# Kernel tuning notes

Measured on AMD Instinct MI355X. Metric: run time of the kernel, lower is better.

## Reference

```python
import jax, jax.numpy as jnp
import numpy as np

G, NPG, HID, NLAYERS, MAXZ, K = 256, 128, 256, 3, 1000, 30
N = G * NPG          # 32768 nodes
E = N * 16           # 524288 edges
TOTAL_DIM = HID * NLAYERS + 1  # 769


def setup_inputs():
    key = jax.random.key(0)
    ks = jax.random.split(key, 12)
    z = jax.random.randint(ks[0], (N,), 0, MAXZ)
    edge_index = jax.random.randint(ks[1], (2, E), 0, N)
    batch = jnp.arange(N) // NPG  # contiguous equal-size graphs
    emb = jax.random.normal(ks[2], (MAXZ, HID), jnp.float32)
    s = 1.0 / np.sqrt(HID)
    gcn_w = jax.random.normal(ks[3], (NLAYERS, HID, HID), jnp.float32) * s
    gcn_b = jnp.zeros((NLAYERS, HID), jnp.float32)
    gcn_w_last = jax.random.normal(ks[4], (HID, 1), jnp.float32) * s
    gcn_b_last = jnp.zeros((1,), jnp.float32)
    conv1_w = jax.random.normal(ks[5], (16, 1, 5), jnp.float32) * (1.0 / np.sqrt(5))
    conv1_b = jnp.zeros((16,), jnp.float32)
    conv2_w = jax.random.normal(ks[6], (32, 16, 5), jnp.float32) * (1.0 / np.sqrt(80))
    conv2_b = jnp.zeros((32,), jnp.float32)
    kd = K * TOTAL_DIM            # 23070
    flat = 32 * ((kd - 4) // 2 - 4)  # 368928
    lin1_w = jax.random.normal(ks[7], (128, flat), jnp.float32) * (1.0 / np.sqrt(flat))
    lin1_b = jnp.zeros((128,), jnp.float32)
    lin2_w = jax.random.normal(ks[8], (1, 128), jnp.float32) * (1.0 / np.sqrt(128))
    lin2_b = jnp.zeros((1,), jnp.float32)
    return dict(z=z, edge_index=edge_index, batch=batch, emb=emb, gcn_w=gcn_w,
                gcn_b=gcn_b, gcn_w_last=gcn_w_last, gcn_b_last=gcn_b_last,
                conv1_w=conv1_w, conv1_b=conv1_b, conv2_w=conv2_w, conv2_b=conv2_b,
                lin1_w=lin1_w, lin1_b=lin1_b, lin2_w=lin2_w, lin2_b=lin2_b)


def reference(z, edge_index, batch, emb, gcn_w, gcn_b, gcn_w_last, gcn_b_last,
              conv1_w, conv1_b, conv2_w, conv2_b, lin1_w, lin1_b, lin2_w, lin2_b):
    src, dst = edge_index[0], edge_index[1]
    # GCNConv normalization with self-loops: D^{-1/2}(A+I)D^{-1/2}
    deg = 1.0 + jax.ops.segment_sum(jnp.ones((E,), jnp.float32), dst, num_segments=N)
    dinv = jax.lax.rsqrt(deg)
    enorm = dinv[src] * dinv[dst]   # per-edge norm
    snorm = 1.0 / deg               # self-loop norm

    def gcn(x, W, b):
        xw = x @ W
        agg = jax.ops.segment_sum(enorm[:, None] * xw[src], dst, num_segments=N)
        return agg + snorm[:, None] * xw + b

    x = emb[z]
    xs = []
    for i in range(NLAYERS):
        x = jnp.tanh(gcn(x, gcn_w[i], gcn_b[i]))
        xs.append(x)
    xs.append(jnp.tanh(gcn(x, gcn_w_last, gcn_b_last)))
    h = jnp.concatenate(xs, axis=-1)  # [N, TOTAL_DIM]

    # global_sort_pool: per-graph descending sort by last channel, keep top-k
    hg = h.reshape(G, NPG, TOTAL_DIM)
    order = jnp.argsort(-hg[:, :, -1], axis=1)
    hg = jnp.take_along_axis(hg, order[:, :, None], axis=1)[:, :K]
    p = hg.reshape(G, 1, K * TOTAL_DIM)

    dn = ('NCH', 'OIH', 'NCH')
    c = jax.lax.conv_general_dilated(p, conv1_w, (1,), 'VALID', dimension_numbers=dn)
    c = jax.nn.relu(c + conv1_b[None, :, None])
    c = jax.lax.reduce_window(c, -jnp.inf, jax.lax.max, (1, 1, 2), (1, 1, 2), 'VALID')
    c = jax.lax.conv_general_dilated(c, conv2_w, (1,), 'VALID', dimension_numbers=dn)
    c = jax.nn.relu(c + conv2_b[None, :, None])
    f = c.reshape(G, -1)
    f = jax.nn.relu(f @ lin1_w.T + lin1_b)
    return (f @ lin2_w.T + lin2_b).reshape(-1)
```

## Files before the change

kernel.cpp:

```cpp
#include <hip/hip_runtime.h>

#define NN      32768
#define EE      524288
#define GG      256
#define NPG     128
#define HID     256
#define KTOP    30
#define TD      769
#define HSTR    772
#define PLEN    23070
#define C1LEN   23066
#define POOLLEN 11533
#define C2LEN   11529
#define FLAT    368928
#define L1_KRANGE 512
#define L1_KS   721

#define SWZ(c) ((c) + 4 * ((c) >> 5))

__global__ __launch_bounds__(256) void k_deg(const int* __restrict__ dst, int* __restrict__ deg_cnt) {
    int e = blockIdx.x * 256 + threadIdx.x;
    atomicAdd(&deg_cnt[dst[e]], 1);
}

__global__ __launch_bounds__(256) void k_norm(const int* __restrict__ deg_cnt,
                                              float* __restrict__ dinv, float* __restrict__ snorm) {
    int n = blockIdx.x * 256 + threadIdx.x;
    float dg = 1.0f + (float)deg_cnt[n];
    dinv[n] = rsqrtf(dg);
    snorm[n] = 1.0f / dg;
}

__global__ __launch_bounds__(1024) void k_scan(const int* __restrict__ deg_cnt, int* __restrict__ row_start) {
    __shared__ int sA[1024];
    int t = threadIdx.x;
    int base = t * 32;
    int s = 0;
    for (int i = 0; i < 32; i++) s += deg_cnt[base + i];
    sA[t] = s;
    __syncthreads();
    for (int off = 1; off < 1024; off <<= 1) {
        int v = (t >= off) ? sA[t - off] : 0;
        __syncthreads();
        sA[t] += v;
        __syncthreads();
    }
    int run = sA[t] - s;
    for (int i = 0; i < 32; i++) { row_start[base + i] = run; run += deg_cnt[base + i]; }
}

__global__ __launch_bounds__(256) void k_csrfill(const int* __restrict__ src, const int* __restrict__ dst,
                                                 const int* __restrict__ row_start, int* __restrict__ fill,
                                                 const float* __restrict__ dinv,
                                                 int* __restrict__ csr_src, float* __restrict__ csr_w) {
    int e = blockIdx.x * 256 + threadIdx.x;
    int s = src[e], d = dst[e];
    int pos = row_start[d] + atomicAdd(&fill[d], 1);
    csr_src[pos] = s;
    csr_w[pos] = dinv[s] * dinv[d];
}

__global__ __launch_bounds__(256) void k_embed(const int* __restrict__ z, const float* __restrict__ emb,
                                               float* __restrict__ x) {
    int i = blockIdx.x * 256 + threadIdx.x;
    int n = i >> 6, l = i & 63;
    ((float4*)x)[(size_t)n * 64 + l] = ((const float4*)emb)[(size_t)z[n] * 64 + l];
}

__global__ __launch_bounds__(256) void k_w2t(const float* __restrict__ w2, float* __restrict__ w2t_g) {
    for (int i = threadIdx.x; i < 2560; i += 256)
        w2t_g[i] = w2[(i & 31) * 80 + (i >> 5)];
}

__global__ __launch_bounds__(256) void k_gemm_gcn(const float* __restrict__ A, const float* __restrict__ B,
                                                  float* __restrict__ C) {
    __shared__ float As[16][132];
    __shared__ float Bs[16][140];
    int m0 = blockIdx.x * 128;
    int n0 = blockIdx.y * 128;
    int tid = threadIdx.x;
    int ty = tid >> 4, tx = tid & 15;
    float acc[8][8] = {};
    for (int k0 = 0; k0 < 256; k0 += 16) {
        {
            int m = tid >> 2, kq = (tid & 3) * 4;
            #pragma unroll
            for (int r = 0; r < 2; r++) {
                float4 v = *(const float4*)&A[(size_t)(m0 + m + 64 * r) * 256 + k0 + kq];
                As[kq + 0][m + 64 * r] = v.x;
                As[kq + 1][m + 64 * r] = v.y;
                As[kq + 2][m + 64 * r] = v.z;
                As[kq + 3][m + 64 * r] = v.w;
            }
            int n = (tid & 31) * 4, kk = tid >> 5;
            #pragma unroll
            for (int r = 0; r < 2; r++) {
                float4 v = *(const float4*)&B[(size_t)(k0 + kk + 8 * r) * 256 + n0 + n];
                *(float4*)&Bs[kk + 8 * r][SWZ(n)] = v;
            }
        }
        __syncthreads();
        #pragma unroll
        for (int k = 0; k < 16; k++) {
            float a[8], b[8];
            *(float4*)&a[0] = *(float4*)&As[k][ty * 8];
            *(float4*)&a[4] = *(float4*)&As[k][ty * 8 + 4];
            *(float4*)&b[0] = *(float4*)&Bs[k][SWZ(tx * 8)];
            *(float4*)&b[4] = *(float4*)&Bs[k][SWZ(tx * 8 + 4)];
            #pragma unroll
            for (int i = 0; i < 8; i++)
                #pragma unroll
                for (int j = 0; j < 8; j++) acc[i][j] += a[i] * b[j];
        }
        __syncthreads();
    }
    #pragma unroll
    for (int i = 0; i < 8; i++) {
        int m = m0 + ty * 8 + i;
        float4 v0 = make_float4(acc[i][0], acc[i][1], acc[i][2], acc[i][3]);
        float4 v1 = make_float4(acc[i][4], acc[i][5], acc[i][6], acc[i][7]);
        *(float4*)&C[(size_t)m * 256 + n0 + tx * 8] = v0;
        *(float4*)&C[(size_t)m * 256 + n0 + tx * 8 + 4] = v1;
    }
}

__global__ __launch_bounds__(256) void k_agg(const float* __restrict__ xw, const int* __restrict__ row_start,
                                             const int* __restrict__ deg_cnt, const int* __restrict__ csr_src,
                                             const float* __restrict__ csr_w, const float* __restrict__ snorm,
                                             const float* __restrict__ bias, float* __restrict__ xn,
                                             float* __restrict__ h, int hoff,
                                             const float* __restrict__ wl, float* __restrict__ xwl) {
    int d = blockIdx.x * 4 + (threadIdx.x >> 6);
    int l = threadIdx.x & 63;
    float4 v = ((const float4*)xw)[(size_t)d * 64 + l];
    float sn = snorm[d];
    float4 acc = make_float4(sn * v.x, sn * v.y, sn * v.z, sn * v.w);
    int st = row_start[d], cnt = deg_cnt[d];
    for (int j = 0; j < cnt; j++) {
        int s = csr_src[st + j];
        float w = csr_w[st + j];
        float4 u = ((const float4*)xw)[(size_t)s * 64 + l];
        acc.x += w * u.x; acc.y += w * u.y; acc.z += w * u.z; acc.w += w * u.w;
    }
    float4 b = ((const float4*)bias)[l];
    acc.x = tanhf(acc.x + b.x);
    acc.y = tanhf(acc.y + b.y);
    acc.z = tanhf(acc.z + b.z);
    acc.w = tanhf(acc.w + b.w);
    ((float4*)xn)[(size_t)d * 64 + l] = acc;
    *(float4*)&h[(size_t)d * HSTR + hoff + l * 4] = acc;
    if (wl != nullptr) {
        float4 w4 = ((const float4*)wl)[l];
        float s = acc.x * w4.x + acc.y * w4.y + acc.z * w4.z + acc.w * w4.w;
        #pragma unroll
        for (int off = 32; off; off >>= 1) s += __shfl_down(s, off, 64);
        if (l == 0) xwl[d] = s;
    }
}

__global__ __launch_bounds__(256) void k_agg_last(const float* __restrict__ xwl, const int* __restrict__ row_start,
                                                  const int* __restrict__ deg_cnt, const int* __restrict__ csr_src,
                                                  const float* __restrict__ csr_w, const float* __restrict__ snorm,
                                                  const float* __restrict__ blast, float* __restrict__ h) {
    int d = blockIdx.x * 256 + threadIdx.x;
    float acc = snorm[d] * xwl[d];
    int st = row_start[d], cnt = deg_cnt[d];
    for (int j = 0; j < cnt; j++) acc += csr_w[st + j] * xwl[csr_src[st + j]];
    h[(size_t)d * HSTR + 768] = tanhf(acc + blast[0]);
}

__global__ __launch_bounds__(128) void k_sort_gather(const float* __restrict__ h, float* __restrict__ P) {
    __shared__ float kk[128];
    __shared__ int ii[128];
    int g = blockIdx.x, t = threadIdx.x;
    kk[t] = h[(size_t)(g * 128 + t) * HSTR + 768];
    ii[t] = t;
    __syncthreads();
    for (int size = 2; size <= 128; size <<= 1) {
        for (int stride = size >> 1; stride > 0; stride >>= 1) {
            int p = t ^ stride;
            if (p > t) {
                float ka = kk[t], kbv = kk[p];
                int ia = ii[t], ib = ii[p];
                bool aFirst = (ka > kbv) || (ka == kbv && ia < ib);
                bool asc = (t & size) == 0;
                if (asc != aFirst) { kk[t] = kbv; kk[p] = ka; ii[t] = ib; ii[p] = ia; }
            }
            __syncthreads();
        }
    }
    float* Pg = P + (size_t)g * PLEN;
    for (int r = 0; r < KTOP; r++) {
        const float* srcp = h + (size_t)(g * 128 + ii[r]) * HSTR;
        for (int c = t; c < TD; c += 128) Pg[(size_t)r * TD + c] = srcp[c];
    }
}

#define JT 128
#define CONV_T 4
__global__ __launch_bounds__(256) void k_conv(const float* __restrict__ P,
                                              const float* __restrict__ w1, const float* __restrict__ b1,
                                              const float* __restrict__ w2t_g, const float* __restrict__ b2,
                                              float* __restrict__ f) {
    __shared__ float sle[136];
    __shared__ float slo[136];
    __shared__ float pool[16][136];
    __shared__ float w2t[80][33];
    __shared__ float outs[32][133];
    __shared__ float w1s[16][5];
    __shared__ float b1s[16];
    __shared__ float b2s[32];
    int g = blockIdx.x;
    int tid = threadIdx.x;
    const float* Pg = P + (size_t)g * PLEN;
    for (int i = tid; i < 2560; i += 256) w2t[i >> 5][i & 31] = w2t_g[i];
    for (int i = tid; i < 80; i += 256) w1s[i / 5][i % 5] = w1[i];
    if (tid < 16) b1s[tid] = b1[tid];
    if (tid < 32) b2s[tid] = b2[tid];

    int c2 = tid & 31;
    int jg = tid >> 5;
    size_t fg = (size_t)g * FLAT;

    for (int tt = 0; tt < CONV_T; tt++) {
        int j0 = (blockIdx.y * CONV_T + tt) * JT;
        if (j0 >= C2LEN) break;
        __syncthreads();
        for (int i = tid; i < 268; i += 256) {
            float v = Pg[min(2 * j0 + i, PLEN - 1)];
            if (i & 1) slo[i >> 1] = v; else sle[i >> 1] = v;
        }
        __syncthreads();
        for (int i = tid; i < 16 * 132; i += 256) {
            int c1 = i / 132, t = i % 132;
            float e0 = sle[t], o0 = slo[t], e1 = sle[t + 1], o1 = slo[t + 1], e2 = sle[t + 2], o2 = slo[t + 2];
            float u0 = w1s[c1][0], u1 = w1s[c1][1], u2 = w1s[c1][2], u3 = w1s[c1][3], u4 = w1s[c1][4];
            float a = b1s[c1] + u0 * e0 + u1 * o0 + u2 * e1 + u3 * o1 + u4 * e2;
            float b = b1s[c1] + u0 * o0 + u1 * e1 + u2 * o1 + u3 * e2 + u4 * o2;
            pool[c1][t] = fmaxf(fmaxf(a, b), 0.0f);
        }
        __syncthreads();
        float acc[16];
        float bb = b2s[c2];
        #pragma unroll
        for (int jj = 0; jj < 16; jj++) acc[jj] = bb;
        int jbase = jg * 16;
        for (int c1 = 0; c1 < 16; c1++) {
            float p[20];
            #pragma unroll
            for (int q = 0; q < 5; q++) {
                float4 v = *(float4*)&pool[c1][jbase + q * 4];
                p[q * 4 + 0] = v.x; p[q * 4 + 1] = v.y; p[q * 4 + 2] = v.z; p[q * 4 + 3] = v.w;
            }
            float wk[5];
            #pragma unroll
            for (int k = 0; k < 5; k++) wk[k] = w2t[c1 * 5 + k][c2];
            #pragma unroll
            for (int k = 0; k < 5; k++)
                #pragma unroll
                for (int jj = 0; jj < 16; jj++) acc[jj] += wk[k] * p[jj + k];
        }
        #pragma unroll
        for (int jj = 0; jj < 16; jj++) outs[c2][jbase + jj] = fmaxf(acc[jj], 0.0f);
        __syncthreads();
        for (int it = 0; it < 16; it++) {
            int i = tid + it * 256;
            int cc = i >> 7, j = (i & 127) + j0;
            if (j < C2LEN) f[fg + (size_t)cc * C2LEN + j] = outs[cc][i & 127];
        }
    }
}

__global__ __launch_bounds__(256) void k_lin1(const float* __restrict__ f, const float* __restrict__ W,
                                              float* __restrict__ partial) {
    __shared__ float As[16][132];
    __shared__ float Bs[16][140];
    int m0 = blockIdx.x * 128;
    int ks = blockIdx.y;
    int kbase = ks * L1_KRANGE;
    int kend = min(kbase + L1_KRANGE, FLAT);
    int tid = threadIdx.x;
    int ty = tid >> 4, tx = tid & 15;
    float acc[8][8] = {};
    for (int k0 = kbase; k0 < kend; k0 += 16) {
        {
            int m = tid >> 2, kq = (tid & 3) * 4;
            #pragma unroll
            for (int r = 0; r < 2; r++) {
                float4 v = *(const float4*)&f[(size_t)(m0 + m + 64 * r) * FLAT + k0 + kq];
                As[kq + 0][m + 64 * r] = v.x;
                As[kq + 1][m + 64 * r] = v.y;
                As[kq + 2][m + 64 * r] = v.z;
                As[kq + 3][m + 64 * r] = v.w;
            }
            int n = tid >> 1, kq2 = (tid & 1) * 8;
            int swn = SWZ(n);
            #pragma unroll
            for (int r = 0; r < 2; r++) {
                int k = kq2 + r * 4;
                float4 v = *(const float4*)&W[(size_t)n * FLAT + k0 + k];
                Bs[k + 0][swn] = v.x; Bs[k + 1][swn] = v.y; Bs[k + 2][swn] = v.z; Bs[k + 3][swn] = v.w;
            }
        }
        __syncthreads();
        #pragma unroll
        for (int k = 0; k < 16; k++) {
            float a[8], b[8];
            *(float4*)&a[0] = *(float4*)&As[k][ty * 8];
            *(float4*)&a[4] = *(float4*)&As[k][ty * 8 + 4];
            *(float4*)&b[0] = *(float4*)&Bs[k][SWZ(tx * 8)];
            *(float4*)&b[4] = *(float4*)&Bs[k][SWZ(tx * 8 + 4)];
            #pragma unroll
            for (int i = 0; i < 8; i++)
                #pragma unroll
                for (int j = 0; j < 8; j++) acc[i][j] += a[i] * b[j];
        }
        __syncthreads();
    }
    #pragma unroll
    for (int i = 0; i < 8; i++) {
        int m = m0 + ty * 8 + i;
        float4 v0 = make_float4(acc[i][0], acc[i][1], acc[i][2], acc[i][3]);
        float4 v1 = make_float4(acc[i][4], acc[i][5], acc[i][6], acc[i][7]);
        *(float4*)&partial[((size_t)ks * 256 + m) * 128 + tx * 8] = v0;
        *(float4*)&partial[((size_t)ks * 256 + m) * 128 + tx * 8 + 4] = v1;
    }
}

__global__ __launch_bounds__(128) void k_reduce(const float* __restrict__ partial, const float* __restrict__ lb1,
                                                const float* __restrict__ lw2, const float* __restrict__ lb2,
                                                float* __restrict__ out) {
    int g = blockIdx.x, o = threadIdx.x;
    float s0 = 0.0f, s1 = 0.0f, s2 = 0.0f, s3 = 0.0f;
    int ks = 0;
    for (; ks + 4 <= L1_KS; ks += 4) {
        s0 += partial[((size_t)(ks + 0) * 256 + g) * 128 + o];
        s1 += partial[((size_t)(ks + 1) * 256 + g) * 128 + o];
        s2 += partial[((size_t)(ks + 2) * 256 + g) * 128 + o];
        s3 += partial[((size_t)(ks + 3) * 256 + g) * 128 + o];
    }
    for (; ks < L1_KS; ks++) s0 += partial[((size_t)ks * 256 + g) * 128 + o];
    float s = (s0 + s1) + (s2 + s3);
    float v = fmaxf(s + lb1[o], 0.0f) * lw2[o];
    #pragma unroll
    for (int off = 32; off; off >>= 1) v += __shfl_down(v, off, 64);
    __shared__ float red[2];
    if ((threadIdx.x & 63) == 0) red[threadIdx.x >> 6] = v;
    __syncthreads();
    if (threadIdx.x == 0) out[g] = red[0] + red[1] + lb2[0];
}

extern "C" void kernel_launch(void* const* d_in, const int* in_sizes, int n_in,
                              void* d_out, int out_size, void* d_ws, size_t ws_size,
                              hipStream_t stream) {
    const int*   z     = (const int*)d_in[0];
    const int*   ei    = (const int*)d_in[1];
    const int*   srcv  = ei;
    const int*   dstv  = ei + EE;
    const float* emb   = (const float*)d_in[3];
    const float* gcnw  = (const float*)d_in[4];
    const float* gcnb  = (const float*)d_in[5];
    const float* wlast = (const float*)d_in[6];
    const float* blast = (const float*)d_in[7];
    const float* w1    = (const float*)d_in[8];
    const float* b1    = (const float*)d_in[9];
    const float* w2    = (const float*)d_in[10];
    const float* b2    = (const float*)d_in[11];
    const float* l1w   = (const float*)d_in[12];
    const float* l1b   = (const float*)d_in[13];
    const float* l2w   = (const float*)d_in[14];
    const float* l2b   = (const float*)d_in[15];
    float* out = (float*)d_out;

    char* base = (char*)d_ws;
    const size_t FB = ((size_t)GG * FLAT * 4 + 511) & ~(size_t)511;
    float* fbuf = (float*)base;
    char* p = base;
    auto alloc = [&](size_t bytes) { void* r = (void*)p; p += (bytes + 511) & ~(size_t)511; return r; };
    int*   deg_cnt = (int*)  alloc((size_t)NN * 4);
    int*   fill    = (int*)  alloc((size_t)NN * 4);
    int*   rowst   = (int*)  alloc((size_t)NN * 4);
    int*   csr_src = (int*)  alloc((size_t)EE * 4);
    float* csr_w   = (float*)alloc((size_t)EE * 4);
    float* dinv    = (float*)alloc((size_t)NN * 4);
    float* snorm   = (float*)alloc((size_t)NN * 4);
    float* xA      = (float*)alloc((size_t)NN * 256 * 4);
    float* xB      = (float*)alloc((size_t)NN * 256 * 4);
    float* xw      = (float*)alloc((size_t)NN * 256 * 4);
    float* h       = (float*)alloc((size_t)NN * HSTR * 4);
    float* xwl     = (float*)alloc((size_t)NN * 4);
    float* P       = (float*)(base + FB);
    float* partial = (float*)(base + FB + (((size_t)GG * PLEN * 4 + 511) & ~(size_t)511));
    float* w2t_g   = partial + (size_t)L1_KS * 256 * 128;
    (void)ws_size; (void)in_sizes; (void)n_in; (void)out_size;

    hipMemsetAsync(deg_cnt, 0, (size_t)NN * 4, stream);
    hipMemsetAsync(fill,    0, (size_t)NN * 4, stream);

    k_deg    <<<EE / 256, 256, 0, stream>>>(dstv, deg_cnt);
    k_norm   <<<NN / 256, 256, 0, stream>>>(deg_cnt, dinv, snorm);
    k_scan   <<<1, 1024, 0, stream>>>(deg_cnt, rowst);
    k_csrfill<<<EE / 256, 256, 0, stream>>>(srcv, dstv, rowst, fill, dinv, csr_src, csr_w);
    k_embed  <<<NN * 64 / 256, 256, 0, stream>>>(z, emb, xA);
    k_w2t    <<<1, 256, 0, stream>>>(w2, w2t_g);

    float* xc = xA;
    float* xn = xB;
    for (int layer = 0; layer < 3; layer++) {
        k_gemm_gcn<<<dim3(NN / 128, 2), 256, 0, stream>>>(xc, gcnw + (size_t)layer * 65536, xw);
        const float* wl = (layer == 2) ? wlast : nullptr;
        k_agg<<<NN / 4, 256, 0, stream>>>(xw, rowst, deg_cnt, csr_src, csr_w, snorm,
                                          gcnb + layer * 256, xn, h, layer * 256, wl, xwl);
        float* t = xc; xc = xn; xn = t;
    }
    k_agg_last<<<NN / 256, 256, 0, stream>>>(xwl, rowst, deg_cnt, csr_src, csr_w, snorm, blast, h);

    k_sort_gather<<<GG, 128, 0, stream>>>(h, P);

    const int ntiles = (C2LEN + JT - 1) / JT;
    k_conv<<<dim3(GG, (ntiles + CONV_T - 1) / CONV_T), 256, 0, stream>>>(P, w1, b1, w2t_g, b2, fbuf);

    k_lin1  <<<dim3(2, L1_KS), 256, 0, stream>>>(fbuf, l1w, partial);
    k_reduce<<<GG, 128, 0, stream>>>(partial, l1b, l2w, l2b, out);
}
```

Measured before the change: 1.472 ms.

## Merge lin1 M-tiles into one 512-thread block with register prefetch

The lin1 split-K GEMM now uses one 512-thread block per K slice that covers all 256 graph rows, where before two 256-thread blocks each covered 128 rows. Each slice of the large lin1 weight matrix is therefore read once instead of twice. The global loads for the next 16-wide K step are also issued into registers before the current step's compute, so load latency overlaps the FMAs. In exchange the grid has half as many blocks, shared memory per block grows, and register pressure rises from the prefetch registers.

Result: no change. 1.491 ms (+1.3%).

```diff
diff --git a/kernel.cpp b/kernel.cpp
--- a/kernel.cpp
+++ b/kernel.cpp
@@ -271,45 +271,45 @@
     }
 }
 
-__global__ __launch_bounds__(256) void k_lin1(const float* __restrict__ f, const float* __restrict__ W,
+__global__ __launch_bounds__(512) void k_lin1(const float* __restrict__ f, const float* __restrict__ W,
                                               float* __restrict__ partial) {
-    __shared__ float As[16][132];
+    __shared__ float As[16][260];
     __shared__ float Bs[16][140];
-    int m0 = blockIdx.x * 128;
-    int ks = blockIdx.y;
+    int ks = blockIdx.x;
     int kbase = ks * L1_KRANGE;
     int kend = min(kbase + L1_KRANGE, FLAT);
     int tid = threadIdx.x;
     int ty = tid >> 4, tx = tid & 15;
+    int arow = tid >> 1, akq = (tid & 1) * 8;
+    int brow = tid >> 2, bkq = (tid & 3) * 4;
+    int swb = SWZ(brow);
+    const float* fA = &f[(size_t)arow * FLAT + kbase + akq];
+    const float* wB = &W[(size_t)brow * FLAT + kbase + bkq];
+    float4 a0 = *(const float4*)fA;
+    float4 a1 = *(const float4*)(fA + 4);
+    float4 b0 = *(const float4*)wB;
     float acc[8][8] = {};
     for (int k0 = kbase; k0 < kend; k0 += 16) {
-        {
-            int m = tid >> 2, kq = (tid & 3) * 4;
-            #pragma unroll
-            for (int r = 0; r < 2; r++) {
-                float4 v = *(const float4*)&f[(size_t)(m0 + m + 64 * r) * FLAT + k0 + kq];
-                As[kq + 0][m + 64 * r] = v.x;
-                As[kq + 1][m + 64 * r] = v.y;
-                As[kq + 2][m + 64 * r] = v.z;
-                As[kq + 3][m + 64 * r] = v.w;
-            }
-            int n = tid >> 1, kq2 = (tid & 1) * 8;
-            int swn = SWZ(n);
-            #pragma unroll
-            for (int r = 0; r < 2; r++) {
-                int k = kq2 + r * 4;
-                float4 v = *(const float4*)&W[(size_t)n * FLAT + k0 + k];
-                Bs[k + 0][swn] = v.x; Bs[k + 1][swn] = v.y; Bs[k + 2][swn] = v.z; Bs[k + 3][swn] = v.w;
-            }
-        }
-        __syncthreads();
+        As[akq + 0][arow] = a0.x; As[akq + 1][arow] = a0.y;
+        As[akq + 2][arow] = a0.z; As[akq + 3][arow] = a0.w;
+        As[akq + 4][arow] = a1.x; As[akq + 5][arow] = a1.y;
+        As[akq + 6][arow] = a1.z; As[akq + 7][arow] = a1.w;
+        Bs[bkq + 0][swb] = b0.x; Bs[bkq + 1][swb] = b0.y;
+        Bs[bkq + 2][swb] = b0.z; Bs[bkq + 3][swb] = b0.w;
+        __syncthreads();
+        if (k0 + 16 < kend) {
+            fA += 16; wB += 16;
+            a0 = *(const float4*)fA;
+            a1 = *(const float4*)(fA + 4);
+            b0 = *(const float4*)wB;
+        }
         #pragma unroll
         for (int k = 0; k < 16; k++) {
             float a[8], b[8];
             *(float4*)&a[0] = *(float4*)&As[k][ty * 8];
             *(float4*)&a[4] = *(float4*)&As[k][ty * 8 + 4];
             *(float4*)&b[0] = *(float4*)&Bs[k][SWZ(tx * 8)];
-            *(float4*)&b[4] = *(float4*)&Bs[k][SWZ(tx * 8 + 4)];
+            *(float4*)&b[4] = *(float4*)&Bs[k][SWZ(tx * 8) + 4];
             #pragma unroll
             for (int i = 0; i < 8; i++)
                 #pragma unroll
@@ -319,7 +319,7 @@
     }
     #pragma unroll
     for (int i = 0; i < 8; i++) {
-        int m = m0 + ty * 8 + i;
+        int m = ty * 8 + i;
         float4 v0 = make_float4(acc[i][0], acc[i][1], acc[i][2], acc[i][3]);
         float4 v1 = make_float4(acc[i][4], acc[i][5], acc[i][6], acc[i][7]);
         *(float4*)&partial[((size_t)ks * 256 + m) * 128 + tx * 8] = v0;
@@ -420,6 +420,6 @@
     const int ntiles = (C2LEN + JT - 1) / JT;
     k_conv<<<dim3(GG, (ntiles + CONV_T - 1) / CONV_T), 256, 0, stream>>>(P, w1, b1, w2t_g, b2, fbuf);
 
-    k_lin1  <<<dim3(2, L1_KS), 256, 0, stream>>>(fbuf, l1w, partial);
+    k_lin1  <<<dim3(L1_KS), 512, 0, stream>>>(fbuf, l1w, partial);
     k_reduce<<<GG, 128, 0, stream>>>(partial, l1b, l2w, l2b, out);
 }
```
